# Kernel tuning notes

Measured on AMD Instinct MI355X. Metric: run time of the kernel, lower is better.

The kernel has to match this reference:

```python
import jax, jax.numpy as jnp
import numpy as np

B, H, S, Dh = 8, 16, 1028, 64
G = 32
L2 = (2 * G - 1) ** 2  # 3969 relative-position entries
HID = 32
R_VAL = 4  # register-token cutoff


def setup_inputs() -> dict:
    key = jax.random.key(0)
    ks = jax.random.split(key, 7)
    return {
        "q": jax.random.normal(ks[0], (B, H, S, Dh), jnp.float32),
        "k": jax.random.normal(ks[1], (B, H, S, Dh), jnp.float32),
        "v": jax.random.normal(ks[2], (B, H, S, Dh), jnp.float32),
        # normalized log-spaced relative coords in [-1, 1], Swin-v2 style
        "rel_table": jax.random.uniform(ks[3], (L2, 2), jnp.float32, -1.0, 1.0),
        "W1": jax.random.normal(ks[4], (2, HID), jnp.float32) * 0.1,
        "b1": jnp.zeros((HID,), jnp.float32),
        "W2": jax.random.normal(ks[5], (HID, H), jnp.float32) * 0.02,
        "idx_table": jax.random.randint(ks[6], (S, S), 0, L2, jnp.int32),
        "R": R_VAL,
    }


def reference(q, k, v, rel_table, W1, b1, W2, idx_table, R):
    # CPB MLP: Linear(2->hid) + exact GELU + Linear(hid->H, no bias)
    bt = jax.nn.gelu(rel_table @ W1 + b1, approximate=False) @ W2  # [L2, H]
    # gather per-(q,kv) bias, move head axis front -> [H, S, S]
    bias = jnp.transpose(bt[idx_table], (2, 0, 1))
    pos = jnp.arange(S) >= R
    has_bias = pos[:, None] & pos[None, :]  # [S, S]
    scale = Dh ** -0.5
    scores = jnp.einsum('bhqd,bhkd->bhqk', q, k) * scale  # [B,H,S,S]
    scores = scores + jnp.where(has_bias, bias, 0.0)[None]
    p = jax.nn.softmax(scores, axis=-1)
    return jnp.einsum('bhqk,bhkd->bhqd', p, v)
```

## Files before the change

### kernel.cpp

```cpp
#include <hip/hip_runtime.h>
#include <hip/hip_bf16.h>

#define S_LEN 1028
#define DH 64
#define NHEAD 16
#define NBATCH 8
#define L2N 3969
#define HIDN 32
#define KVB 64
#define NKT 17
#define NQT 17
#define TILE_E 4096

typedef __bf16 bf16x8 __attribute__((ext_vector_type(8)));
typedef __bf16 bf16x4 __attribute__((ext_vector_type(4)));
typedef float f32x4 __attribute__((ext_vector_type(4)));

__device__ __forceinline__ bf16x8 cvt_bf16x8(float4 a, float4 b) {
  bf16x8 r;
  r[0] = (__bf16)a.x; r[1] = (__bf16)a.y; r[2] = (__bf16)a.z; r[3] = (__bf16)a.w;
  r[4] = (__bf16)b.x; r[5] = (__bf16)b.y; r[6] = (__bf16)b.z; r[7] = (__bf16)b.w;
  return r;
}

__device__ __forceinline__ f32x4 mfma16(bf16x8 a, bf16x8 b, f32x4 c) {
  return __builtin_amdgcn_mfma_f32_16x16x32_bf16(a, b, c, 0, 0, 0);
}

#define GLD16(gsrc, ldst)                                                     \
  __builtin_amdgcn_global_load_lds(                                           \
      (const __attribute__((address_space(1))) void*)(gsrc),                  \
      (__attribute__((address_space(3))) void*)(ldst), 16, 0, 0)

__global__ void cpb_table_lh(const float* __restrict__ rel,
                             const float* __restrict__ W1,
                             const float* __restrict__ b1,
                             const float* __restrict__ W2,
                             float* __restrict__ bt) {
  int i = blockIdx.x * blockDim.x + threadIdx.x;
  if (i >= L2N) return;
  float x = rel[2 * i], y = rel[2 * i + 1];
  float acc[NHEAD];
#pragma unroll
  for (int h = 0; h < NHEAD; ++h) acc[h] = 0.f;
#pragma unroll
  for (int j = 0; j < HIDN; ++j) {
    float t = fmaf(x, W1[j], fmaf(y, W1[HIDN + j], b1[j]));
    float g = 0.5f * t * (1.f + erff(t * 0.70710678118654752f));
#pragma unroll
    for (int h = 0; h < NHEAD; ++h) acc[h] = fmaf(g, W2[j * NHEAD + h], acc[h]);
  }
#pragma unroll
  for (int h = 0; h < NHEAD; ++h) bt[(size_t)i * NHEAD + h] = acc[h];
}

__global__ void bias_expand(const int* __restrict__ idx,
                            const float* __restrict__ bt,
                            const int* __restrict__ Rp,
                            __bf16* __restrict__ bias) {
  const int qrow = blockIdx.x;
  const int R = Rp[0];
  const bool qok = (qrow >= R);
  for (int k = threadIdx.x; k < S_LEN; k += blockDim.x) {
    const int l = idx[(size_t)qrow * S_LEN + k];
    const bool on = qok && (k >= R);
    const float4* btv = (const float4*)bt + (size_t)l * 4;
    float va[16];
    *(float4*)&va[0]  = btv[0];
    *(float4*)&va[4]  = btv[1];
    *(float4*)&va[8]  = btv[2];
    *(float4*)&va[12] = btv[3];
#pragma unroll
    for (int h = 0; h < NHEAD; ++h)
      bias[(size_t)h * S_LEN * S_LEN + (size_t)qrow * S_LEN + k] =
          on ? (__bf16)va[h] : (__bf16)0.f;
  }
}

__global__ __launch_bounds__(256) void kv_pack(const float* __restrict__ kg,
                                               const float* __restrict__ vg,
                                               __bf16* __restrict__ Kb,
                                               __bf16* __restrict__ Vb) {
  const int it = blockIdx.x, bh = blockIdx.y;
  const int kb = it * KVB;
  const int tid = threadIdx.x;
  const float* kp = kg + (size_t)bh * S_LEN * DH;
  const float* vp = vg + (size_t)bh * S_LEN * DH;
  __bf16* kout = Kb + ((size_t)bh * NKT + it) * TILE_E;
  __bf16* vout = Vb + ((size_t)bh * NKT + it) * TILE_E;

  for (int i = tid; i < 512; i += 256) {
    const int rho = i >> 3, gx = i & 7;
    const int e = ((rho & 15) << 2) | (rho >> 4);
    const int key = kb + e;
    const int gsrc = gx ^ (rho & 7);
    float4 a = {0.f, 0.f, 0.f, 0.f}, b = {0.f, 0.f, 0.f, 0.f};
    if (key < S_LEN) {
      a = *(const float4*)(kp + (size_t)key * DH + gsrc * 8);
      b = *(const float4*)(kp + (size_t)key * DH + gsrc * 8 + 4);
    }
    *(bf16x8*)(kout + (size_t)rho * 64 + gx * 8) = cvt_bf16x8(a, b);
  }

  __shared__ float vt[64][68];
  for (int i = tid; i < 1024; i += 256) {
    const int row = i >> 4, c4 = i & 15;
    const int key = kb + row;
    float4 a = {0.f, 0.f, 0.f, 0.f};
    if (key < S_LEN) a = *(const float4*)(vp + (size_t)key * DH + c4 * 4);
    *(float4*)&vt[row][c4 * 4] = a;
  }
  __syncthreads();
  for (int i = tid; i < 512; i += 256) {
    const int d = i >> 3, gx = i & 7;
    const int kg8 = (gx ^ (d & 7)) * 8;
    bf16x8 o;
#pragma unroll
    for (int j = 0; j < 8; ++j) o[j] = (__bf16)vt[kg8 + j][d];
    *(bf16x8*)(vout + (size_t)d * 64 + gx * 8) = o;
  }
}

__global__ __launch_bounds__(256, 4) void flex_attn_v3(
    const float* __restrict__ qg, const __bf16* __restrict__ Kb,
    const __bf16* __restrict__ Vb, const __bf16* __restrict__ biasG,
    float* __restrict__ out) {
  const int b = blockIdx.z, h = blockIdx.y, qt = blockIdx.x;
  const int bh = b * NHEAD + h;
  const int tid = threadIdx.x;
  const int wave = tid >> 6, lane = tid & 63;
  const int g = lane >> 4, m = lane & 15;

  __shared__ __align__(16) __bf16 Kt[2][KVB][64];
  __shared__ __align__(16) __bf16 Vt[2][DH][64];
  __shared__ __align__(16) __bf16 Pl[4][16][64];

  const __bf16* KbT = Kb + (size_t)bh * NKT * TILE_E;
  const __bf16* VbT = Vb + (size_t)bh * NKT * TILE_E;
  const __bf16* bp = biasG + (size_t)h * S_LEN * S_LEN;
  const float* qp = qg + (size_t)bh * S_LEN * DH;

  const int qrow = qt * 64 + wave * 16 + m;
  bf16x8 qf[2];
#pragma unroll
  for (int dc = 0; dc < 2; ++dc) {
    float4 a = {0.f, 0.f, 0.f, 0.f}, bb = {0.f, 0.f, 0.f, 0.f};
    if (qrow < S_LEN) {
      a = *(const float4*)(qp + (size_t)qrow * DH + dc * 32 + g * 8);
      bb = *(const float4*)(qp + (size_t)qrow * DH + dc * 32 + g * 8 + 4);
    }
    a.x *= 0.125f; a.y *= 0.125f; a.z *= 0.125f; a.w *= 0.125f;
    bb.x *= 0.125f; bb.y *= 0.125f; bb.z *= 0.125f; bb.w *= 0.125f;
    qf[dc] = cvt_bf16x8(a, bb);
  }

  const int qb4 = qt * 64 + wave * 16 + g * 4;
  const __bf16* brow[4];
#pragma unroll
  for (int r = 0; r < 4; ++r) {
    int qq = qb4 + r; if (qq > S_LEN - 1) qq = S_LEN - 1;
    brow[r] = bp + (size_t)qq * S_LEN;
  }

  f32x4 acc_o[4];
#pragma unroll
  for (int t = 0; t < 4; ++t) acc_o[t] = (f32x4){0.f, 0.f, 0.f, 0.f};
  float lsum[4] = {0.f, 0.f, 0.f, 0.f};

  const int sw_m = (m & 7) << 3;
  const int lo16 = lane * 8;

  {
    const __bf16* gk = KbT + wave * 1024 + lo16;
    const __bf16* gv = VbT + wave * 1024 + lo16;
    __bf16* lk = &Kt[0][0][0] + wave * 1024;
    __bf16* lv = &Vt[0][0][0] + wave * 1024;
    GLD16(gk, lk); GLD16(gk + 512, lk + 512);
    GLD16(gv, lv); GLD16(gv + 512, lv + 512);
  }

  for (int it = 0; it < NKT; ++it) {
    const int buf = it & 1;
    const int kb = it * KVB;
    const int kk = kb + 4 * m;
    const bool kvalid = (kk < S_LEN);
    const float kvf = kvalid ? 1.f : 0.f;

    bf16x4 bias4[4];
#pragma unroll
    for (int r = 0; r < 4; ++r) {
      bf16x4 z; z[0] = (__bf16)0.f; z[1] = (__bf16)0.f; z[2] = (__bf16)0.f; z[3] = (__bf16)0.f;
      bias4[r] = kvalid ? *(const bf16x4*)(brow[r] + kk) : z;
    }

    __builtin_amdgcn_s_barrier();

    {
      const int nit = (it + 1 < NKT) ? it + 1 : 0;
      const __bf16* gk = KbT + (size_t)nit * TILE_E + wave * 1024 + lo16;
      const __bf16* gv = VbT + (size_t)nit * TILE_E + wave * 1024 + lo16;
      __bf16* lk = &Kt[buf ^ 1][0][0] + wave * 1024;
      __bf16* lv = &Vt[buf ^ 1][0][0] + wave * 1024;
      GLD16(gk, lk); GLD16(gk + 512, lk + 512);
      GLD16(gv, lv); GLD16(gv + 512, lv + 512);
    }

    asm volatile("s_waitcnt vmcnt(8)" ::: "memory");
    __builtin_amdgcn_s_barrier();
    __builtin_amdgcn_sched_barrier(0);

    f32x4 sc[4];
#pragma unroll
    for (int c = 0; c < 4; ++c) {
      f32x4 a = (f32x4){0.f, 0.f, 0.f, 0.f};
#pragma unroll
      for (int dc = 0; dc < 2; ++dc) {
        bf16x8 kf = *(bf16x8*)&Kt[buf][c * 16 + m][(dc * 32 + g * 8) ^ sw_m];
        a = mfma16(qf[dc], kf, a);
      }
      sc[c] = a;
    }

#pragma unroll
    for (int r = 0; r < 4; ++r) {
      float p0 = __expf(sc[0][r] + (float)bias4[r][0]) * kvf;
      float p1 = __expf(sc[1][r] + (float)bias4[r][1]) * kvf;
      float p2 = __expf(sc[2][r] + (float)bias4[r][2]) * kvf;
      float p3 = __expf(sc[3][r] + (float)bias4[r][3]) * kvf;
      lsum[r] += (p0 + p1) + (p2 + p3);
      bf16x4 pb;
      pb[0] = (__bf16)p0; pb[1] = (__bf16)p1; pb[2] = (__bf16)p2; pb[3] = (__bf16)p3;
      const int row = g * 4 + r;
      *(bf16x4*)&Pl[wave][row][(4 * m) ^ ((row & 7) << 3)] = pb;
    }

#pragma unroll
    for (int kc = 0; kc < 2; ++kc) {
      bf16x8 pf = *(bf16x8*)&Pl[wave][m][(kc * 32 + g * 8) ^ sw_m];
#pragma unroll
      for (int t = 0; t < 4; ++t) {
        bf16x8 vf = *(bf16x8*)&Vt[buf][t * 16 + m][(kc * 32 + g * 8) ^ sw_m];
        acc_o[t] = mfma16(pf, vf, acc_o[t]);
      }
    }
  }

#pragma unroll
  for (int r = 0; r < 4; ++r) {
    float s = lsum[r];
    s += __shfl_xor(s, 1);
    s += __shfl_xor(s, 2);
    s += __shfl_xor(s, 4);
    s += __shfl_xor(s, 8);
    const int qq = qb4 + r;
    if (qq >= S_LEN) continue;
    const float inv = 1.f / s;
    float* op = out + (((size_t)bh) * S_LEN + qq) * DH;
#pragma unroll
    for (int t = 0; t < 4; ++t) op[t * 16 + m] = acc_o[t][r] * inv;
  }
}

__global__ __launch_bounds__(256, 4) void flex_attn_fast(
    const float* __restrict__ qg, const float* __restrict__ kg,
    const float* __restrict__ vg, const __bf16* __restrict__ biasG,
    float* __restrict__ out) {
  const int b = blockIdx.z, h = blockIdx.y, qt = blockIdx.x;
  const int tid = threadIdx.x;
  const int wave = tid >> 6, lane = tid & 63;
  const int g = lane >> 4, m = lane & 15;

  __shared__ __align__(16) __bf16 Kt[KVB][72];
  __shared__ __align__(16) __bf16 Vt[DH][72];
  __shared__ __align__(16) __bf16 Pl[4][16][72];

  const size_t base = ((size_t)(b * NHEAD + h)) * S_LEN * DH;
  const float* qp = qg + base;
  const float* kp = kg + base;
  const float* vp = vg + base;
  const __bf16* bp = biasG + (size_t)h * S_LEN * S_LEN;

  const int qrow = qt * 64 + wave * 16 + m;
  bf16x8 qf[2];
#pragma unroll
  for (int dc = 0; dc < 2; ++dc) {
    float4 a = {0.f, 0.f, 0.f, 0.f}, bb = {0.f, 0.f, 0.f, 0.f};
    if (qrow < S_LEN) {
      a = *(const float4*)(qp + (size_t)qrow * DH + dc * 32 + g * 8);
      bb = *(const float4*)(qp + (size_t)qrow * DH + dc * 32 + g * 8 + 4);
    }
    a.x *= 0.125f; a.y *= 0.125f; a.z *= 0.125f; a.w *= 0.125f;
    bb.x *= 0.125f; bb.y *= 0.125f; bb.z *= 0.125f; bb.w *= 0.125f;
    qf[dc] = cvt_bf16x8(a, bb);
  }

  f32x4 acc_o[4];
#pragma unroll
  for (int t = 0; t < 4; ++t) acc_o[t] = (f32x4){0.f, 0.f, 0.f, 0.f};
  float mrow[4], lrow[4];
#pragma unroll
  for (int r = 0; r < 4; ++r) { mrow[r] = -1e30f; lrow[r] = 0.f; }

  const int qb4 = qt * 64 + wave * 16 + g * 4;
  const int eK = wave * 16 + (lane >> 2);
  const int rowK = ((eK & 3) << 4) | (eK >> 2);
  const int colK = (lane & 3) * 16;

  for (int it = 0; it < NKT; ++it) {
    const int kb = it * KVB;
    __syncthreads();
    {
      const int krow = kb + eK;
      float4 a0 = {0,0,0,0}, a1 = {0,0,0,0}, a2 = {0,0,0,0}, a3 = {0,0,0,0};
      if (krow < S_LEN) {
        const float* src = kp + (size_t)krow * DH + colK;
        a0 = *(const float4*)(src);
        a1 = *(const float4*)(src + 4);
        a2 = *(const float4*)(src + 8);
        a3 = *(const float4*)(src + 12);
      }
      *(bf16x8*)&Kt[rowK][colK] = cvt_bf16x8(a0, a1);
      *(bf16x8*)&Kt[rowK][colK + 8] = cvt_bf16x8(a2, a3);
    }
    {
      bf16x8 p0, p1;
#pragma unroll
      for (int t = 0; t < 8; ++t) {
        const int kr = kb + wave * 16 + t;
        p0[t] = (kr < S_LEN) ? (__bf16)vp[(size_t)kr * DH + lane] : (__bf16)0.f;
      }
#pragma unroll
      for (int t = 0; t < 8; ++t) {
        const int kr = kb + wave * 16 + 8 + t;
        p1[t] = (kr < S_LEN) ? (__bf16)vp[(size_t)kr * DH + lane] : (__bf16)0.f;
      }
      *(bf16x8*)&Vt[lane][wave * 16] = p0;
      *(bf16x8*)&Vt[lane][wave * 16 + 8] = p1;
    }

    const int kk = kb + 4 * m;
    const bool kvalid = (kk < S_LEN);
    bf16x4 bias4[4];
#pragma unroll
    for (int r = 0; r < 4; ++r) {
      const int qq = (qb4 + r < S_LEN) ? qb4 + r : S_LEN - 1;
      bf16x4 z; z[0] = (__bf16)0.f; z[1] = (__bf16)0.f; z[2] = (__bf16)0.f; z[3] = (__bf16)0.f;
      bias4[r] = kvalid ? *(const bf16x4*)(bp + (size_t)qq * S_LEN + kk) : z;
    }

    __syncthreads();

    f32x4 sc[4];
#pragma unroll
    for (int c = 0; c < 4; ++c) {
      f32x4 a = (f32x4){0.f, 0.f, 0.f, 0.f};
#pragma unroll
      for (int dc = 0; dc < 2; ++dc) {
        bf16x8 kf = *(bf16x8*)&Kt[c * 16 + m][dc * 32 + g * 8];
        a = mfma16(qf[dc], kf, a);
      }
      sc[c] = a;
    }

#pragma unroll
    for (int r = 0; r < 4; ++r) {
      float s[4];
#pragma unroll
      for (int c = 0; c < 4; ++c)
        s[c] = kvalid ? sc[c][r] + (float)bias4[r][c] : -1e30f;
      float mx = fmaxf(fmaxf(s[0], s[1]), fmaxf(s[2], s[3]));
      mx = fmaxf(mx, __shfl_xor(mx, 1));
      mx = fmaxf(mx, __shfl_xor(mx, 2));
      mx = fmaxf(mx, __shfl_xor(mx, 4));
      mx = fmaxf(mx, __shfl_xor(mx, 8));
      const float mnew = fmaxf(mrow[r], mx);
      const float alpha = __expf(mrow[r] - mnew);
      float p0 = __expf(s[0] - mnew), p1 = __expf(s[1] - mnew);
      float p2 = __expf(s[2] - mnew), p3 = __expf(s[3] - mnew);
      float sum = (p0 + p1) + (p2 + p3);
      sum += __shfl_xor(sum, 1);
      sum += __shfl_xor(sum, 2);
      sum += __shfl_xor(sum, 4);
      sum += __shfl_xor(sum, 8);
      lrow[r] = lrow[r] * alpha + sum;
      mrow[r] = mnew;
      bf16x4 pb;
      pb[0] = (__bf16)p0; pb[1] = (__bf16)p1; pb[2] = (__bf16)p2; pb[3] = (__bf16)p3;
      *(bf16x4*)&Pl[wave][g * 4 + r][4 * m] = pb;
#pragma unroll
      for (int t = 0; t < 4; ++t) acc_o[t][r] *= alpha;
    }

#pragma unroll
    for (int kc = 0; kc < 2; ++kc) {
      bf16x8 pf = *(bf16x8*)&Pl[wave][m][kc * 32 + g * 8];
#pragma unroll
      for (int t = 0; t < 4; ++t) {
        bf16x8 vf = *(bf16x8*)&Vt[t * 16 + m][kc * 32 + g * 8];
        acc_o[t] = mfma16(pf, vf, acc_o[t]);
      }
    }
  }

#pragma unroll
  for (int r = 0; r < 4; ++r) {
    const int qq = qb4 + r;
    if (qq >= S_LEN) continue;
    const float inv = 1.f / lrow[r];
    float* op = out + (((size_t)(b * NHEAD + h)) * S_LEN + qq) * DH;
#pragma unroll
    for (int t = 0; t < 4; ++t) op[t * 16 + m] = acc_o[t][r] * inv;
  }
}

extern "C" void kernel_launch(void* const* d_in, const int* in_sizes, int n_in,
                              void* d_out, int out_size, void* d_ws, size_t ws_size,
                              hipStream_t stream) {
  const float* q = (const float*)d_in[0];
  const float* k = (const float*)d_in[1];
  const float* v = (const float*)d_in[2];
  const float* rel = (const float*)d_in[3];
  const float* W1 = (const float*)d_in[4];
  const float* b1 = (const float*)d_in[5];
  const float* W2 = (const float*)d_in[6];
  const int* idx = (const int*)d_in[7];
  const int* Rp = (const int*)d_in[8];
  float* out = (float*)d_out;

  const size_t bt_bytes = 1u << 18;
  const size_t bias_bytes = (size_t)NHEAD * S_LEN * S_LEN * 2;
  const size_t kv_bytes = (size_t)NBATCH * NHEAD * NKT * TILE_E * 2;

  if (ws_size >= bt_bytes + bias_bytes + 2 * kv_bytes) {
    float* bt = (float*)d_ws;
    __bf16* bias = (__bf16*)((char*)d_ws + bt_bytes);
    __bf16* Kb = (__bf16*)((char*)d_ws + bt_bytes + bias_bytes);
    __bf16* Vb = (__bf16*)((char*)d_ws + bt_bytes + bias_bytes + kv_bytes);
    cpb_table_lh<<<dim3((L2N + 255) / 256), dim3(256), 0, stream>>>(rel, W1, b1, W2, bt);
    bias_expand<<<dim3(S_LEN), dim3(256), 0, stream>>>(idx, bt, Rp, bias);
    kv_pack<<<dim3(NKT, NBATCH * NHEAD), dim3(256), 0, stream>>>(k, v, Kb, Vb);
    flex_attn_v3<<<dim3(NQT, NHEAD, NBATCH), dim3(256), 0, stream>>>(q, Kb, Vb, bias, out);
  } else {
    float* bt = (float*)d_ws;
    __bf16* bias = (__bf16*)((char*)d_ws + bt_bytes);
    cpb_table_lh<<<dim3((L2N + 255) / 256), dim3(256), 0, stream>>>(rel, W1, b1, W2, bt);
    bias_expand<<<dim3(S_LEN), dim3(256), 0, stream>>>(idx, bt, Rp, bias);
    flex_attn_fast<<<dim3(NQT, NHEAD, NBATCH), dim3(256), 0, stream>>>(q, k, v, bias, out);
  }
}
```

Baseline: 279.8 us.

## Fold log2e into bias and Q, use exp2, peel masked tile, coalesce bias writes

The bias table is pre-scaled by log2(e) and Q by 0.125*log2(e), so the softmax can use the native exp2 instruction. The bias is loaded straight into the MFMA accumulator, which removes the separate add. The last partial KV tile is peeled so the 16 full tiles skip the validity checks, and that loop is unrolled by 2. bias_expand now stages each row in LDS so every head is written as coalesced 16-byte stores instead of scattered 2-byte stores. Rounding the pre-scaled bias to bf16 shifts precision slightly.

After: 276.7 us. Within noise of the previous version (-1.1%).

```diff
diff --git a/kernel.cpp b/kernel.cpp
--- a/kernel.cpp
+++ b/kernel.cpp
@@ -11,6 +11,7 @@
 #define NKT 17
 #define NQT 17
 #define TILE_E 4096
+#define LOG2E 1.4426950408889634f
 
 typedef __bf16 bf16x8 __attribute__((ext_vector_type(8)));
 typedef __bf16 bf16x4 __attribute__((ext_vector_type(4)));
@@ -25,6 +26,14 @@
 
 __device__ __forceinline__ f32x4 mfma16(bf16x8 a, bf16x8 b, f32x4 c) {
   return __builtin_amdgcn_mfma_f32_16x16x32_bf16(a, b, c, 0, 0, 0);
+}
+
+__device__ __forceinline__ float exp2_fast(float x) {
+#if __has_builtin(__builtin_amdgcn_exp2f)
+  return __builtin_amdgcn_exp2f(x);
+#else
+  return __expf(x * 0.6931471805599453f);
+#endif
 }
 
 #define GLD16(gsrc, ldst)                                                     \
@@ -54,14 +63,18 @@
   for (int h = 0; h < NHEAD; ++h) bt[(size_t)i * NHEAD + h] = acc[h];
 }
 
-__global__ void bias_expand(const int* __restrict__ idx,
-                            const float* __restrict__ bt,
-                            const int* __restrict__ Rp,
-                            __bf16* __restrict__ bias) {
+__global__ __launch_bounds__(256) void bias_expand2(const int* __restrict__ idx,
+                                                    const float* __restrict__ bt,
+                                                    const int* __restrict__ Rp,
+                                                    __bf16* __restrict__ bias) {
   const int qrow = blockIdx.x;
   const int R = Rp[0];
   const bool qok = (qrow >= R);
-  for (int k = threadIdx.x; k < S_LEN; k += blockDim.x) {
+  const int tid = threadIdx.x;
+  __shared__ __align__(16) __bf16 strip[NHEAD][264];
+
+  for (int k0 = 0; k0 < 1024; k0 += 256) {
+    const int k = k0 + tid;
     const int l = idx[(size_t)qrow * S_LEN + k];
     const bool on = qok && (k >= R);
     const float4* btv = (const float4*)bt + (size_t)l * 4;
@@ -72,8 +85,26 @@
     *(float4*)&va[12] = btv[3];
 #pragma unroll
     for (int h = 0; h < NHEAD; ++h)
-      bias[(size_t)h * S_LEN * S_LEN + (size_t)qrow * S_LEN + k] =
-          on ? (__bf16)va[h] : (__bf16)0.f;
+      strip[h][tid] = on ? (__bf16)(va[h] * LOG2E) : (__bf16)0.f;
+    __syncthreads();
+    {
+      const int h = tid >> 4, kg = tid & 15;
+      bf16x8 w0 = *(bf16x8*)&strip[h][kg * 16];
+      bf16x8 w1 = *(bf16x8*)&strip[h][kg * 16 + 8];
+      __bf16* dst = bias + (size_t)h * S_LEN * S_LEN + (size_t)qrow * S_LEN + k0 + kg * 16;
+      *(bf16x8*)dst = w0;
+      *(bf16x8*)(dst + 8) = w1;
+    }
+    __syncthreads();
+  }
+  if (tid < 64) {
+    const int kt = tid & 3, h = tid >> 2;
+    const int k = 1024 + kt;
+    const int l = idx[(size_t)qrow * S_LEN + k];
+    const bool on = qok && (k >= R);
+    const float v = bt[(size_t)l * NHEAD + h];
+    bias[(size_t)h * S_LEN * S_LEN + (size_t)qrow * S_LEN + k] =
+        on ? (__bf16)(v * LOG2E) : (__bf16)0.f;
   }
 }
 
@@ -121,7 +152,73 @@
   }
 }
 
-__global__ __launch_bounds__(256, 4) void flex_attn_v3(
+#define TILE_STEP(ITC, MASKED) do {                                           \
+    const int buf_ = (ITC) & 1;                                               \
+    const int kk_ = (ITC) * KVB + 4 * m;                                      \
+    bf16x4 bias4_[4];                                                         \
+    _Pragma("unroll")                                                         \
+    for (int r = 0; r < 4; ++r) {                                             \
+      bf16x4 z_; z_[0] = (__bf16)0.f; z_[1] = (__bf16)0.f;                    \
+      z_[2] = (__bf16)0.f; z_[3] = (__bf16)0.f;                               \
+      bias4_[r] = (!(MASKED) || kk_ < S_LEN)                                  \
+                      ? *(const bf16x4*)(brow[r] + kk_) : z_;                 \
+    }                                                                         \
+    __builtin_amdgcn_s_barrier();                                             \
+    {                                                                         \
+      const int nit_ = ((ITC) + 1 < NKT) ? (ITC) + 1 : 0;                     \
+      const __bf16* gk_ = KbT + (size_t)nit_ * TILE_E + wave * 1024 + lo16;   \
+      const __bf16* gv_ = VbT + (size_t)nit_ * TILE_E + wave * 1024 + lo16;   \
+      __bf16* lk_ = &Kt[buf_ ^ 1][0][0] + wave * 1024;                        \
+      __bf16* lv_ = &Vt[buf_ ^ 1][0][0] + wave * 1024;                        \
+      GLD16(gk_, lk_); GLD16(gk_ + 512, lk_ + 512);                           \
+      GLD16(gv_, lv_); GLD16(gv_ + 512, lv_ + 512);                           \
+    }                                                                         \
+    asm volatile("s_waitcnt vmcnt(8)" ::: "memory");                          \
+    __builtin_amdgcn_s_barrier();                                             \
+    __builtin_amdgcn_sched_barrier(0);                                        \
+    f32x4 sc_[4];                                                             \
+    _Pragma("unroll")                                                         \
+    for (int c = 0; c < 4; ++c) {                                             \
+      f32x4 a_;                                                               \
+      _Pragma("unroll")                                                       \
+      for (int r = 0; r < 4; ++r) a_[r] = (float)bias4_[r][c];                \
+      _Pragma("unroll")                                                       \
+      for (int dc = 0; dc < 2; ++dc) {                                        \
+        bf16x8 kf_ = *(bf16x8*)&Kt[buf_][c * 16 + m][(dc * 32 + g * 8) ^ sw_m]; \
+        a_ = mfma16(qf[dc], kf_, a_);                                         \
+      }                                                                       \
+      sc_[c] = a_;                                                            \
+    }                                                                         \
+    _Pragma("unroll")                                                         \
+    for (int r = 0; r < 4; ++r) {                                             \
+      float p0_ = exp2_fast(sc_[0][r]);                                       \
+      float p1_ = exp2_fast(sc_[1][r]);                                       \
+      float p2_ = exp2_fast(sc_[2][r]);                                       \
+      float p3_ = exp2_fast(sc_[3][r]);                                       \
+      if (MASKED) {                                                           \
+        const float kvf_ = (kk_ < S_LEN) ? 1.f : 0.f;                         \
+        lsum[r] += kvf_ * ((p0_ + p1_) + (p2_ + p3_));                        \
+      } else {                                                                \
+        lsum[r] += (p0_ + p1_) + (p2_ + p3_);                                 \
+      }                                                                       \
+      bf16x4 pb_;                                                             \
+      pb_[0] = (__bf16)p0_; pb_[1] = (__bf16)p1_;                             \
+      pb_[2] = (__bf16)p2_; pb_[3] = (__bf16)p3_;                             \
+      const int row_ = g * 4 + r;                                             \
+      *(bf16x4*)&Pl[wave][row_][(4 * m) ^ ((row_ & 7) << 3)] = pb_;           \
+    }                                                                         \
+    _Pragma("unroll")                                                         \
+    for (int kc = 0; kc < 2; ++kc) {                                          \
+      bf16x8 pf_ = *(bf16x8*)&Pl[wave][m][(kc * 32 + g * 8) ^ sw_m];          \
+      _Pragma("unroll")                                                       \
+      for (int t = 0; t < 4; ++t) {                                           \
+        bf16x8 vf_ = *(bf16x8*)&Vt[buf_][t * 16 + m][(kc * 32 + g * 8) ^ sw_m]; \
+        acc_o[t] = mfma16(pf_, vf_, acc_o[t]);                                \
+      }                                                                       \
+    }                                                                         \
+  } while (0)
+
+__global__ __launch_bounds__(256, 4) void flex_attn_v4(
     const float* __restrict__ qg, const __bf16* __restrict__ Kb,
     const __bf16* __restrict__ Vb, const __bf16* __restrict__ biasG,
     float* __restrict__ out) {
@@ -141,6 +238,7 @@
   const float* qp = qg + (size_t)bh * S_LEN * DH;
 
   const int qrow = qt * 64 + wave * 16 + m;
+  const float qs = 0.125f * LOG2E;
   bf16x8 qf[2];
 #pragma unroll
   for (int dc = 0; dc < 2; ++dc) {
@@ -149,8 +247,8 @@
       a = *(const float4*)(qp + (size_t)qrow * DH + dc * 32 + g * 8);
       bb = *(const float4*)(qp + (size_t)qrow * DH + dc * 32 + g * 8 + 4);
     }
-    a.x *= 0.125f; a.y *= 0.125f; a.z *= 0.125f; a.w *= 0.125f;
-    bb.x *= 0.125f; bb.y *= 0.125f; bb.z *= 0.125f; bb.w *= 0.125f;
+    a.x *= qs; a.y *= qs; a.z *= qs; a.w *= qs;
+    bb.x *= qs; bb.y *= qs; bb.z *= qs; bb.w *= qs;
     qf[dc] = cvt_bf16x8(a, bb);
   }
 
@@ -179,71 +277,11 @@
     GLD16(gv, lv); GLD16(gv + 512, lv + 512);
   }
 
-  for (int it = 0; it < NKT; ++it) {
-    const int buf = it & 1;
-    const int kb = it * KVB;
-    const int kk = kb + 4 * m;
-    const bool kvalid = (kk < S_LEN);
-    const float kvf = kvalid ? 1.f : 0.f;
-
-    bf16x4 bias4[4];
-#pragma unroll
-    for (int r = 0; r < 4; ++r) {
-      bf16x4 z; z[0] = (__bf16)0.f; z[1] = (__bf16)0.f; z[2] = (__bf16)0.f; z[3] = (__bf16)0.f;
-      bias4[r] = kvalid ? *(const bf16x4*)(brow[r] + kk) : z;
-    }
-
-    __builtin_amdgcn_s_barrier();
-
-    {
-      const int nit = (it + 1 < NKT) ? it + 1 : 0;
-      const __bf16* gk = KbT + (size_t)nit * TILE_E + wave * 1024 + lo16;
-      const __bf16* gv = VbT + (size_t)nit * TILE_E + wave * 1024 + lo16;
-      __bf16* lk = &Kt[buf ^ 1][0][0] + wave * 1024;
-      __bf16* lv = &Vt[buf ^ 1][0][0] + wave * 1024;
-      GLD16(gk, lk); GLD16(gk + 512, lk + 512);
-      GLD16(gv, lv); GLD16(gv + 512, lv + 512);
-    }
-
-    asm volatile("s_waitcnt vmcnt(8)" ::: "memory");
-    __builtin_amdgcn_s_barrier();
-    __builtin_amdgcn_sched_barrier(0);
-
-    f32x4 sc[4];
-#pragma unroll
-    for (int c = 0; c < 4; ++c) {
-      f32x4 a = (f32x4){0.f, 0.f, 0.f, 0.f};
-#pragma unroll
-      for (int dc = 0; dc < 2; ++dc) {
-        bf16x8 kf = *(bf16x8*)&Kt[buf][c * 16 + m][(dc * 32 + g * 8) ^ sw_m];
-        a = mfma16(qf[dc], kf, a);
-      }
-      sc[c] = a;
-    }
-
-#pragma unroll
-    for (int r = 0; r < 4; ++r) {
-      float p0 = __expf(sc[0][r] + (float)bias4[r][0]) * kvf;
-      float p1 = __expf(sc[1][r] + (float)bias4[r][1]) * kvf;
-      float p2 = __expf(sc[2][r] + (float)bias4[r][2]) * kvf;
-      float p3 = __expf(sc[3][r] + (float)bias4[r][3]) * kvf;
-      lsum[r] += (p0 + p1) + (p2 + p3);
-      bf16x4 pb;
-      pb[0] = (__bf16)p0; pb[1] = (__bf16)p1; pb[2] = (__bf16)p2; pb[3] = (__bf16)p3;
-      const int row = g * 4 + r;
-      *(bf16x4*)&Pl[wave][row][(4 * m) ^ ((row & 7) << 3)] = pb;
-    }
-
-#pragma unroll
-    for (int kc = 0; kc < 2; ++kc) {
-      bf16x8 pf = *(bf16x8*)&Pl[wave][m][(kc * 32 + g * 8) ^ sw_m];
-#pragma unroll
-      for (int t = 0; t < 4; ++t) {
-        bf16x8 vf = *(bf16x8*)&Vt[buf][t * 16 + m][(kc * 32 + g * 8) ^ sw_m];
-        acc_o[t] = mfma16(pf, vf, acc_o[t]);
-      }
-    }
-  }
+#pragma unroll 2
+  for (int it = 0; it < 16; ++it) {
+    TILE_STEP(it, false);
+  }
+  TILE_STEP(16, true);
 
 #pragma unroll
   for (int r = 0; r < 4; ++r) {
@@ -281,6 +319,7 @@
   const __bf16* bp = biasG + (size_t)h * S_LEN * S_LEN;
 
   const int qrow = qt * 64 + wave * 16 + m;
+  const float qs = 0.125f * LOG2E;
   bf16x8 qf[2];
 #pragma unroll
   for (int dc = 0; dc < 2; ++dc) {
@@ -289,8 +328,8 @@
       a = *(const float4*)(qp + (size_t)qrow * DH + dc * 32 + g * 8);
       bb = *(const float4*)(qp + (size_t)qrow * DH + dc * 32 + g * 8 + 4);
     }
-    a.x *= 0.125f; a.y *= 0.125f; a.z *= 0.125f; a.w *= 0.125f;
-    bb.x *= 0.125f; bb.y *= 0.125f; bb.z *= 0.125f; bb.w *= 0.125f;
+    a.x *= qs; a.y *= qs; a.z *= qs; a.w *= qs;
+    bb.x *= qs; bb.y *= qs; bb.z *= qs; bb.w *= qs;
     qf[dc] = cvt_bf16x8(a, bb);
   }
 
@@ -374,9 +413,9 @@
       mx = fmaxf(mx, __shfl_xor(mx, 4));
       mx = fmaxf(mx, __shfl_xor(mx, 8));
       const float mnew = fmaxf(mrow[r], mx);
-      const float alpha = __expf(mrow[r] - mnew);
-      float p0 = __expf(s[0] - mnew), p1 = __expf(s[1] - mnew);
-      float p2 = __expf(s[2] - mnew), p3 = __expf(s[3] - mnew);
+      const float alpha = exp2_fast(mrow[r] - mnew);
+      float p0 = exp2_fast(s[0] - mnew), p1 = exp2_fast(s[1] - mnew);
+      float p2 = exp2_fast(s[2] - mnew), p3 = exp2_fast(s[3] - mnew);
       float sum = (p0 + p1) + (p2 + p3);
       sum += __shfl_xor(sum, 1);
       sum += __shfl_xor(sum, 2);
@@ -437,14 +476,14 @@
     __bf16* Kb = (__bf16*)((char*)d_ws + bt_bytes + bias_bytes);
     __bf16* Vb = (__bf16*)((char*)d_ws + bt_bytes + bias_bytes + kv_bytes);
     cpb_table_lh<<<dim3((L2N + 255) / 256), dim3(256), 0, stream>>>(rel, W1, b1, W2, bt);
-    bias_expand<<<dim3(S_LEN), dim3(256), 0, stream>>>(idx, bt, Rp, bias);
+    bias_expand2<<<dim3(S_LEN), dim3(256), 0, stream>>>(idx, bt, Rp, bias);
     kv_pack<<<dim3(NKT, NBATCH * NHEAD), dim3(256), 0, stream>>>(k, v, Kb, Vb);
-    flex_attn_v3<<<dim3(NQT, NHEAD, NBATCH), dim3(256), 0, stream>>>(q, Kb, Vb, bias, out);
+    flex_attn_v4<<<dim3(NQT, NHEAD, NBATCH), dim3(256), 0, stream>>>(q, Kb, Vb, bias, out);
   } else {
     float* bt = (float*)d_ws;
     __bf16* bias = (__bf16*)((char*)d_ws + bt_bytes);
     cpb_table_lh<<<dim3((L2N + 255) / 256), dim3(256), 0, stream>>>(rel, W1, b1, W2, bt);
-    bias_expand<<<dim3(S_LEN), dim3(256), 0, stream>>>(idx, bt, Rp, bias);
+    bias_expand2<<<dim3(S_LEN), dim3(256), 0, stream>>>(idx, bt, Rp, bias);
     flex_attn_fast<<<dim3(NQT, NHEAD, NBATCH), dim3(256), 0, stream>>>(q, k, v, bias, out);
   }
 }
```
